# Optimization experiments

Measured on AMD Instinct MI355X. Metric: run time of the kernel, lower is better.

## Reference

```python
import jax, jax.numpy as jnp
import numpy as np


def setup_inputs() -> dict:
    key = jax.random.key(0)
    k1, k2, k3 = jax.random.split(key, 3)
    B, S, H = 32, 2048, 1024
    hidden = jax.random.normal(k1, (B, H), dtype=jnp.float32)
    encoder_outputs = jax.random.normal(k2, (B, S, H), dtype=jnp.float32)
    W_in = jax.random.normal(k3, (H, H), dtype=jnp.float32) * (1.0 / np.sqrt(H))
    return {"hidden": hidden, "encoder_outputs": encoder_outputs, "W_in": W_in}


def reference(hidden, encoder_outputs, W_in):
    # linear_in: nn.Linear(H, H, bias=False) -> hidden @ W_in.T  [B, H]
    h = hidden @ W_in.T
    # scores: bmm(encoder_outputs [B,S,H], h [B,H,1]) -> [B,S]
    scores = jnp.einsum("bsh,bh->bs", encoder_outputs, h)
    attn_w = jax.nn.softmax(scores, axis=-1)  # [B, S]
    # context: bmm(attn_w [B,1,S], encoder_outputs [B,S,H]) -> [B, H]
    context = jnp.einsum("bs,bsh->bh", attn_w, encoder_outputs)
    return (context, attn_w)
```

## Files before the change

### kernel.cpp

```cpp
#include <hip/hip_runtime.h>
#include <math.h>

constexpr int Bb = 32;
constexpr int Ss = 2048;
constexpr int Hh = 1024;
constexpr int SC = 128;
constexpr int CPB = Ss / SC;
constexpr int NBLK = Bb * CPB;

__global__ __launch_bounds__(256) void gemv_h_kernel(const float* __restrict__ hidden,
                                                     const float* __restrict__ W,
                                                     float* __restrict__ h)
{
    int tid  = threadIdx.x;
    int wave = tid >> 6;
    int lane = tid & 63;
    int i  = blockIdx.x & (Hh - 1);
    int bg = blockIdx.x >> 10;
    int b  = bg * 4 + wave;
    const float4* wr = reinterpret_cast<const float4*>(W + (size_t)i * Hh);
    const float4* hd = reinterpret_cast<const float4*>(hidden + (size_t)b * Hh);
    float d = 0.f;
#pragma unroll
    for (int k = 0; k < 4; ++k) {
        float4 wv = wr[lane + 64 * k];
        float4 hv = hd[lane + 64 * k];
        d += wv.x * hv.x + wv.y * hv.y + wv.z * hv.z + wv.w * hv.w;
    }
#pragma unroll
    for (int off = 32; off > 0; off >>= 1) d += __shfl_xor(d, off, 64);
    if (lane == 0) h[(size_t)b * Hh + i] = d;
}

__global__ __launch_bounds__(256) void attn_partial_kernel(const float* __restrict__ enc,
                                                           const float* __restrict__ h,
                                                           float* __restrict__ scores,
                                                           float* __restrict__ pm,
                                                           float* __restrict__ pl,
                                                           float* __restrict__ pctx)
{
    int blk   = blockIdx.x;
    int b     = blk >> 4;
    int chunk = blk & (CPB - 1);
    int s0    = chunk * SC;
    int tid   = threadIdx.x;
    int wave  = tid >> 6;
    int lane  = tid & 63;

    float4 hf[4];
    const float4* h4 = reinterpret_cast<const float4*>(h + (size_t)b * Hh);
#pragma unroll
    for (int k = 0; k < 4; ++k) hf[k] = h4[lane + 64 * k];

    float m = -INFINITY;
    float l = 0.f;
    float4 ctx[4];
#pragma unroll
    for (int k = 0; k < 4; ++k) ctx[k] = make_float4(0.f, 0.f, 0.f, 0.f);

    const float4* ebase = reinterpret_cast<const float4*>(enc + ((size_t)b * Ss + s0 + wave * 32) * Hh);

#define LOADQ(EV, Q)                                                        \
    {                                                                       \
        _Pragma("unroll")                                                   \
        for (int r = 0; r < 4; ++r) {                                       \
            const float4* e4 = ebase + (size_t)((Q) * 4 + r) * (Hh / 4);    \
            _Pragma("unroll")                                               \
            for (int k = 0; k < 4; ++k) EV[r][k] = e4[lane + 64 * k];       \
        }                                                                   \
    }

#define COMPQ(EV, Q)                                                        \
    {                                                                       \
        float d[4];                                                         \
        _Pragma("unroll")                                                   \
        for (int r = 0; r < 4; ++r) {                                       \
            d[r] = 0.f;                                                     \
            _Pragma("unroll")                                               \
            for (int k = 0; k < 4; ++k)                                     \
                d[r] += EV[r][k].x * hf[k].x + EV[r][k].y * hf[k].y +       \
                        EV[r][k].z * hf[k].z + EV[r][k].w * hf[k].w;        \
        }                                                                   \
        _Pragma("unroll")                                                   \
        for (int off = 32; off > 0; off >>= 1) {                            \
            _Pragma("unroll")                                               \
            for (int r = 0; r < 4; ++r) d[r] += __shfl_xor(d[r], off, 64);  \
        }                                                                   \
        if (lane == 0) {                                                    \
            *reinterpret_cast<float4*>(scores + (size_t)b * Ss + s0 +       \
                                       wave * 32 + 4 * (Q)) =               \
                make_float4(d[0], d[1], d[2], d[3]);                        \
        }                                                                   \
        float mn = fmaxf(fmaxf(fmaxf(d[0], d[1]), fmaxf(d[2], d[3])), m);   \
        if (mn > m) {                                                       \
            float c = __expf(m - mn);                                       \
            l *= c;                                                         \
            _Pragma("unroll")                                               \
            for (int k = 0; k < 4; ++k) {                                   \
                ctx[k].x *= c; ctx[k].y *= c; ctx[k].z *= c; ctx[k].w *= c; \
            }                                                               \
            m = mn;                                                         \
        }                                                                   \
        float p[4];                                                         \
        _Pragma("unroll")                                                   \
        for (int r = 0; r < 4; ++r) p[r] = __expf(d[r] - m);                \
        l += (p[0] + p[1]) + (p[2] + p[3]);                                 \
        _Pragma("unroll")                                                   \
        for (int k = 0; k < 4; ++k) {                                       \
            _Pragma("unroll")                                               \
            for (int r = 0; r < 4; ++r) {                                   \
                ctx[k].x += p[r] * EV[r][k].x;                              \
                ctx[k].y += p[r] * EV[r][k].y;                              \
                ctx[k].z += p[r] * EV[r][k].z;                              \
                ctx[k].w += p[r] * EV[r][k].w;                              \
            }                                                               \
        }                                                                   \
    }

    float4 evA[4][4], evB[4][4];
    LOADQ(evA, 0);
#pragma unroll 1
    for (int qq = 0; qq < 3; ++qq) {
        LOADQ(evB, 2 * qq + 1);
        COMPQ(evA, 2 * qq);
        LOADQ(evA, 2 * qq + 2);
        COMPQ(evB, 2 * qq + 1);
    }
    LOADQ(evB, 7);
    COMPQ(evA, 6);
    COMPQ(evB, 7);
#undef LOADQ
#undef COMPQ

    __shared__ float lds_ctx[4][Hh];
    __shared__ float lds_m[4], lds_l[4];
    float4* ldsrow = reinterpret_cast<float4*>(lds_ctx[wave]);
#pragma unroll
    for (int k = 0; k < 4; ++k) ldsrow[64 * k + lane] = ctx[k];
    if (lane == 0) { lds_m[wave] = m; lds_l[wave] = l; }
    __syncthreads();

    float M = fmaxf(fmaxf(lds_m[0], lds_m[1]), fmaxf(lds_m[2], lds_m[3]));
    float L = 0.f;
    float4 acc = make_float4(0.f, 0.f, 0.f, 0.f);
#pragma unroll
    for (int w = 0; w < 4; ++w) {
        float c = __expf(lds_m[w] - M);
        L += c * lds_l[w];
        float4 v = reinterpret_cast<float4*>(lds_ctx[w])[tid];
        acc.x += c * v.x; acc.y += c * v.y; acc.z += c * v.z; acc.w += c * v.w;
    }
    reinterpret_cast<float4*>(pctx + (size_t)blk * Hh)[tid] = acc;
    if (tid == 0) { pm[blk] = M; pl[blk] = L; }
}

__global__ __launch_bounds__(256) void combine_finish_kernel(const float* __restrict__ pm,
                                                             const float* __restrict__ pl,
                                                             const float* __restrict__ pctx,
                                                             const float* __restrict__ scores,
                                                             float* __restrict__ out_ctx,
                                                             float* __restrict__ attn_out)
{
    int blk = blockIdx.x;
    int tid = threadIdx.x;
    if (blk < 128) {
        int b = blk >> 2;
        int col = (blk & 3) * 256 + tid;
        const float* mrow = pm + (size_t)b * CPB;
        const float* lrow = pl + (size_t)b * CPB;
        float M = -INFINITY;
#pragma unroll
        for (int c = 0; c < CPB; ++c) M = fmaxf(M, mrow[c]);
        float e[CPB];
        float L = 0.f;
#pragma unroll
        for (int c = 0; c < CPB; ++c) {
            e[c] = __expf(mrow[c] - M);
            L += e[c] * lrow[c];
        }
        float acc = 0.f;
#pragma unroll 4
        for (int c = 0; c < CPB; ++c)
            acc += e[c] * pctx[((size_t)b * CPB + c) * Hh + col];
        out_ctx[(size_t)b * Hh + col] = acc / L;
    } else {
        int idx = (blk - 128) * 256 + tid;
        int b = idx >> 11;
        const float* mrow = pm + (size_t)b * CPB;
        const float* lrow = pl + (size_t)b * CPB;
        float M = -INFINITY;
#pragma unroll
        for (int c = 0; c < CPB; ++c) M = fmaxf(M, mrow[c]);
        float L = 0.f;
#pragma unroll
        for (int c = 0; c < CPB; ++c) L += __expf(mrow[c] - M) * lrow[c];
        attn_out[idx] = __expf(scores[idx] - M) / L;
    }
}

extern "C" void kernel_launch(void* const* d_in, const int* in_sizes, int n_in,
                              void* d_out, int out_size, void* d_ws, size_t ws_size,
                              hipStream_t stream) {
    const float* hidden = (const float*)d_in[0];
    const float* enc    = (const float*)d_in[1];
    const float* W_in   = (const float*)d_in[2];

    float* out_ctx  = (float*)d_out;
    float* out_attn = (float*)d_out + Bb * Hh;

    float* ws     = (float*)d_ws;
    float* h      = ws;
    float* scores = ws + 32768;
    float* pm     = ws + 98304;
    float* pl     = ws + 98816;
    float* pctx   = ws + 99328;
    (void)in_sizes; (void)n_in; (void)out_size; (void)ws_size;

    gemv_h_kernel<<<Hh * (Bb / 4), 256, 0, stream>>>(hidden, W_in, h);
    attn_partial_kernel<<<NBLK, 256, 0, stream>>>(enc, h, scores, pm, pl, pctx);
    combine_finish_kernel<<<128 + (Bb * Ss) / 256, 256, 0, stream>>>(pm, pl, pctx, scores,
                                                                     out_ctx, out_attn);
}
```

Measured before the change: 59.84 us.

## Restructure hidden-projection GEMV to one thread per output element

The projection kernel now assigns each thread a full 1024-length dot product for one (batch, output) pair, with 8 outputs × 32 batches per block and 128 blocks total. This removes the wave-level shuffle reduction and the repeated W row fetches across batch groups. In exchange it launches far fewer blocks than there are CUs, serializes 256 iterations per thread, and reads hidden rows with a large per-lane stride.

```diff
diff --git a/kernel.cpp b/kernel.cpp
--- a/kernel.cpp
+++ b/kernel.cpp
@@ -1,5 +1,7 @@
 #include <hip/hip_runtime.h>
 #include <math.h>
+
+typedef float f32x4 __attribute__((ext_vector_type(4)));
 
 constexpr int Bb = 32;
 constexpr int Ss = 2048;
@@ -12,24 +14,20 @@
                                                      const float* __restrict__ W,
                                                      float* __restrict__ h)
 {
-    int tid  = threadIdx.x;
-    int wave = tid >> 6;
-    int lane = tid & 63;
-    int i  = blockIdx.x & (Hh - 1);
-    int bg = blockIdx.x >> 10;
-    int b  = bg * 4 + wave;
-    const float4* wr = reinterpret_cast<const float4*>(W + (size_t)i * Hh);
-    const float4* hd = reinterpret_cast<const float4*>(hidden + (size_t)b * Hh);
-    float d = 0.f;
-#pragma unroll
-    for (int k = 0; k < 4; ++k) {
-        float4 wv = wr[lane + 64 * k];
-        float4 hv = hd[lane + 64 * k];
-        d += wv.x * hv.x + wv.y * hv.y + wv.z * hv.z + wv.w * hv.w;
-    }
-#pragma unroll
-    for (int off = 32; off > 0; off >>= 1) d += __shfl_xor(d, off, 64);
-    if (lane == 0) h[(size_t)b * Hh + i] = d;
+    int t  = threadIdx.x;
+    int b  = t & 31;
+    int di = t >> 5;
+    int i  = blockIdx.x * 8 + di;
+    const f32x4* wr = reinterpret_cast<const f32x4*>(W + (size_t)i * Hh);
+    const f32x4* hd = reinterpret_cast<const f32x4*>(hidden + (size_t)b * Hh);
+    float acc = 0.f;
+#pragma unroll 8
+    for (int k = 0; k < Hh / 4; ++k) {
+        f32x4 wv = wr[k];
+        f32x4 hv = hd[k];
+        acc += wv[0] * hv[0] + wv[1] * hv[1] + wv[2] * hv[2] + wv[3] * hv[3];
+    }
+    h[(size_t)b * Hh + i] = acc;
 }
 
 __global__ __launch_bounds__(256) void attn_partial_kernel(const float* __restrict__ enc,
@@ -216,7 +214,7 @@
     float* pctx   = ws + 99328;
     (void)in_sizes; (void)n_in; (void)out_size; (void)ws_size;
 
-    gemv_h_kernel<<<Hh * (Bb / 4), 256, 0, stream>>>(hidden, W_in, h);
+    gemv_h_kernel<<<Hh / 8, 256, 0, stream>>>(hidden, W_in, h);
     attn_partial_kernel<<<NBLK, 256, 0, stream>>>(enc, h, scores, pm, pl, pctx);
     combine_finish_kernel<<<128 + (Bb * Ss) / 256, 256, 0, stream>>>(pm, pl, pctx, scores,
                                                                      out_ctx, out_attn);
```

New measurement: 92.61 us. 1.55x slower.
